# Kernel optimization log

Hardware: AMD Instinct MI355X
Metric: run time of the kernel (lower is better)

## Reference

```python
import jax, jax.numpy as jnp
import numpy as np

N = 100_000      # nodes
E = 1_600_000    # edges
NG = 512         # graphs in batch
EPS = 1e-5


def _prop(x, src, dst, n, add_self_loops):
    """GCN-normalized sparse propagation: agg_i = sum_{j->i} d_j^-1/2 d_i^-1/2 x_j."""
    ones = jnp.ones(src.shape[0], x.dtype)
    deg = jax.ops.segment_sum(ones, dst, num_segments=n)
    if add_self_loops:
        deg = deg + 1.0
    dinv = jnp.where(deg > 0, jax.lax.rsqrt(jnp.maximum(deg, 1e-12)), 0.0)
    w = dinv[src] * dinv[dst]                       # [E]
    agg = jax.ops.segment_sum(x[src] * w[:, None], dst, num_segments=n)
    if add_self_loops:
        agg = agg + x * (dinv * dinv)[:, None]
    return agg


def setup_inputs() -> dict:
    key = jax.random.key(0)
    ks = jax.random.split(key, 24)
    w = lambda k, s: jax.random.normal(k, s, jnp.float32) * 0.05
    dim = 100
    return {
        "x": jax.random.normal(ks[0], (N, 128), jnp.float32),
        "src": jax.random.randint(ks[1], (E,), 0, N),
        "dst": jax.random.randint(ks[2], (E,), 0, N),
        "batch": jnp.sort(jax.random.randint(ks[3], (N,), 0, NG)),
        # SGConv 1 & 2 (propagate then Linear)
        "W1": w(ks[4], (128, dim)), "b1": jnp.zeros((dim,), jnp.float32),
        "W2": w(ks[5], (dim, dim)), "b2": jnp.zeros((dim,), jnp.float32),
        # BatchNorm1d affine params
        "gamma": jnp.ones((dim,), jnp.float32), "beta": jnp.zeros((dim,), jnp.float32),
        # ARMAConv (num_stacks=1, num_layers=1)
        "Wa_init": w(ks[6], (dim, dim)), "Wa_root": w(ks[7], (dim, dim)),
        "ba": jnp.zeros((dim,), jnp.float32),
        # MLP head
        "Wf1": w(ks[8], (dim, 2 * dim)), "bf1": jnp.zeros((2 * dim,), jnp.float32),
        "Wf2": w(ks[9], (2 * dim, 3 * dim)), "bf2": jnp.zeros((3 * dim,), jnp.float32),
        "Wf3": w(ks[10], (3 * dim, 2 * dim)), "bf3": jnp.zeros((2 * dim,), jnp.float32),
        "Wf4": w(ks[11], (2 * dim, 1)), "bf4": jnp.zeros((1,), jnp.float32),
    }


def reference(x, src, dst, batch, W1, b1, W2, b2, gamma, beta,
              Wa_init, Wa_root, ba, Wf1, bf1, Wf2, bf2, Wf3, bf3, Wf4, bf4):
    n = x.shape[0]
    # SGConv (K=1): propagate with self-loop gcn_norm, then linear; ReLU
    h = jax.nn.relu(_prop(x, src, dst, n, True) @ W1 + b1)
    h = jax.nn.relu(_prop(h, src, dst, n, True) @ W2 + b2)
    # BatchNorm1d (training mode: batch statistics, biased var)
    mu = jnp.mean(h, axis=0)
    var = jnp.mean((h - mu) ** 2, axis=0)
    h = (h - mu) * jax.lax.rsqrt(var + EPS) * gamma + beta
    # ARMAConv (1 stack, 1 layer): ReLU(A_hat (h W_init) + h W_root + b), no self-loops
    a = jax.nn.relu(_prop(h @ Wa_init, src, dst, n, False) + h @ Wa_root + ba)
    # global_add_pool over graph ids
    g = jax.ops.segment_sum(a, batch, num_segments=NG)   # [NG, dim]
    # MLP head
    g = jax.nn.relu(g @ Wf1 + bf1)
    g = jax.nn.relu(g @ Wf2 + bf2)
    g = jax.nn.relu(g @ Wf3 + bf3)
    return g @ Wf4 + bf4
```

## Files before the change

### kernel.cpp

```cpp
#include <hip/hip_runtime.h>
#include <hip/hip_fp16.h>

#define NNODES 100000
#define NEDGES 1600000
#define NGRAPH 512
#define DIM    100
#define DP     128
#define EPSBN  1e-5f
#define NBUK   ((NNODES + 255) >> 8)
#define BINCH  8192

typedef _Float16 half8 __attribute__((ext_vector_type(8)));
typedef float floatx4 __attribute__((ext_vector_type(4)));

__global__ __launch_bounds__(256) void bin_count_kernel(const int* __restrict__ dst,
                                                        int* __restrict__ btotal, int e) {
    __shared__ int lc[NBUK];
    int tid = threadIdx.x;
    int base = blockIdx.x * BINCH;
    int m = e - base; if (m > BINCH) m = BINCH;
    for (int b = tid; b < NBUK; b += 256) lc[b] = 0;
    __syncthreads();
    for (int j = tid; j < m; j += 256)
        atomicAdd(&lc[dst[base + j] >> 8], 1);
    __syncthreads();
    for (int b = tid; b < NBUK; b += 256)
        if (lc[b]) atomicAdd(&btotal[b], lc[b]);
}

__global__ void bucket_scan_kernel(const int* __restrict__ btotal, int* __restrict__ bbase,
                                   int* __restrict__ bcursor, int e,
                                   const int* __restrict__ batch, int* __restrict__ gstart, int n) {
    __shared__ int s[512];
    int tid = threadIdx.x;
    int v = (tid < NBUK) ? btotal[tid] : 0;
    s[tid] = v; __syncthreads();
    for (int o = 1; o < 512; o <<= 1) {
        int t = (tid >= o) ? s[tid - o] : 0;
        __syncthreads();
        s[tid] += t;
        __syncthreads();
    }
    if (tid < NBUK) {
        int base = s[tid] - v;
        bbase[tid] = base;
        bcursor[tid] = base;
    }
    if (tid == 0) bbase[NBUK] = e;

    {
        int g = tid;
        int lo = 0, hi = n;
        while (lo < hi) {
            int mid = (lo + hi) >> 1;
            if (batch[mid] < g) lo = mid + 1; else hi = mid;
        }
        gstart[g] = lo;
        if (g == 0) gstart[NGRAPH] = n;
    }
}

__global__ __launch_bounds__(256) void bin_kernel(
        const int* __restrict__ src, const int* __restrict__ dst,
        int* __restrict__ bcursor, unsigned int* __restrict__ gpairs, int e) {
    __shared__ int2 lpairs[BINCH];
    __shared__ int lcount[NBUK], lstart[NBUK], lcur[NBUK], gbase[NBUK];
    int tid = threadIdx.x;
    int base = blockIdx.x * BINCH;
    int m = e - base; if (m > BINCH) m = BINCH;

    for (int b = tid; b < NBUK; b += 256) lcount[b] = 0;
    __syncthreads();
    for (int j = tid; j < m; j += 256)
        atomicAdd(&lcount[dst[base + j] >> 8], 1);
    __syncthreads();
    if (tid == 0) {
        int acc = 0;
        for (int b = 0; b < NBUK; b++) {
            lstart[b] = acc;
            lcur[b] = acc;
            acc += lcount[b];
        }
    }
    __syncthreads();
    for (int b = tid; b < NBUK; b += 256)
        gbase[b] = atomicAdd(&bcursor[b], lcount[b]);
    for (int j = tid; j < m; j += 256) {
        int s = src[base + j], d = dst[base + j];
        int p = atomicAdd(&lcur[d >> 8], 1);
        lpairs[p] = make_int2(s, d);
    }
    __syncthreads();
    for (int j = tid; j < m; j += 256) {
        int2 pr = lpairs[j];
        int b = pr.y >> 8;
        gpairs[gbase[b] + (j - lstart[b])] =
            ((unsigned int)pr.x << 8) | ((unsigned int)pr.y & 255u);
    }
}

__global__ __launch_bounds__(256) void bucket_build_kernel(
        const unsigned int* __restrict__ gpairs, const int* __restrict__ bbase,
        int* __restrict__ off, int* __restrict__ ssorted,
        float* __restrict__ dsl, float* __restrict__ dnsl, int n, int e) {
    __shared__ int cnt[256];
    __shared__ int sc[256];
    int b = blockIdx.x, tid = threadIdx.x;
    int node0 = b << 8;
    int e0 = bbase[b], e1 = bbase[b + 1];

    cnt[tid] = 0;
    __syncthreads();
    for (int j = e0 + tid; j < e1; j += 256)
        atomicAdd(&cnt[gpairs[j] & 255u], 1);
    __syncthreads();

    int c = cnt[tid];
    sc[tid] = c; __syncthreads();
    for (int o = 1; o < 256; o <<= 1) {
        int t = (tid >= o) ? sc[tid - o] : 0;
        __syncthreads();
        sc[tid] += t;
        __syncthreads();
    }
    int excl = sc[tid] - c;

    int node = node0 + tid;
    if (node < n) {
        off[node] = e0 + excl;
        float cf = (float)c;
        dsl[node] = rsqrtf(cf + 1.0f);
        dnsl[node] = (c > 0) ? rsqrtf(cf) : 0.0f;
    }
    if (b == NBUK - 1 && tid == 0) off[n] = e;

    __syncthreads();
    cnt[tid] = e0 + excl;
    __syncthreads();
    for (int j = e0 + tid; j < e1; j += 256) {
        unsigned int pk = gpairs[j];
        int p = atomicAdd(&cnt[pk & 255u], 1);
        ssorted[p] = (int)(pk >> 8);
    }
}

__global__ void packW4_kernel(const float* __restrict__ W1, const float* __restrict__ W2,
                              const float* __restrict__ W3, const float* __restrict__ W4,
                              _Float16* __restrict__ Wt1, _Float16* __restrict__ Wt2,
                              _Float16* __restrict__ Wt3, _Float16* __restrict__ Wt4,
                              const float* __restrict__ b1, const float* __restrict__ b2,
                              float* __restrict__ b1p, float* __restrict__ b2p,
                              int* __restrict__ btotal, float* __restrict__ bnsum,
                              float* __restrict__ bnsq, __half* __restrict__ buf0zr) {
    if (blockIdx.x == 256) {
        int t = threadIdx.x;
        if (t < 128) {
            b1p[t] = (t < DIM) ? b1[t] : 0.f;
            b2p[t] = (t < DIM) ? b2[t] : 0.f;
            bnsum[t] = 0.f;
            bnsq[t] = 0.f;
        }
        for (int i = t; i < NBUK; i += 256) btotal[i] = 0;
        if (t < 64) ((unsigned int*)buf0zr)[t] = 0u;
        return;
    }
    int which = blockIdx.x >> 6;
    int idx = (blockIdx.x & 63) * 256 + threadIdx.x;
    const float* W = (which == 0) ? W1 : (which == 1) ? W2 : (which == 2) ? W3 : W4;
    _Float16* Wt  = (which == 0) ? Wt1 : (which == 1) ? Wt2 : (which == 2) ? Wt3 : Wt4;
    int K = (which == 0) ? 128 : DIM;
    int j = idx & 7;
    int l = (idx >> 3) & 63;
    int c = idx >> 9;
    int t = c >> 2, k0 = c & 3;
    int nn = t * 16 + (l & 15);
    int k = k0 * 32 + (l >> 4) * 8 + j;
    float v = (k < K && nn < DIM) ? W[k * DIM + nn] : 0.f;
    Wt[idx] = (_Float16)v;
}

__global__ __launch_bounds__(256) void prop_kernel(
        const __half* __restrict__ pre, const int* __restrict__ ssorted,
        const int* __restrict__ off, const float* __restrict__ dinv,
        const float* __restrict__ bias, __half* __restrict__ outH, int n) {
    int wave = (blockIdx.x * blockDim.x + threadIdx.x) >> 6;
    int lane = threadIdx.x & 63;
    if (wave >= n) return;
    int e0 = off[wave], e1 = off[wave + 1];
    int deg = e1 - e0;
    int g = lane >> 4;
    int q = lane & 15;
    const int ZR = n;

    float acc[8];
#pragma unroll
    for (int i = 0; i < 8; i++) acc[i] = 0.f;

    auto addu = [&](uint4 u) {
        float2 f;
        f = __half22float2(*(__half2*)&u.x); acc[0] += f.x; acc[1] += f.y;
        f = __half22float2(*(__half2*)&u.y); acc[2] += f.x; acc[3] += f.y;
        f = __half22float2(*(__half2*)&u.z); acc[4] += f.x; acc[5] += f.y;
        f = __half22float2(*(__half2*)&u.w); acc[6] += f.x; acc[7] += f.y;
    };
    auto rowptr = [&](int s) -> const uint4* {
        return (const uint4*)&pre[(long)s * DP + q * 8];
    };

    for (int base = 0; base < deg; base += 64) {
        int m = deg - base; if (m > 64) m = 64;
        int sidx = (lane < m) ? ssorted[e0 + base + lane] : ZR;
        for (int j = 0; j < m; j += 16) {
            int s0 = __shfl(sidx, j + g);
            int s1 = __shfl(sidx, j + 4 + g);
            int s2 = __shfl(sidx, j + 8 + g);
            int s3 = __shfl(sidx, j + 12 + g);
            uint4 u0 = *rowptr(s0);
            uint4 u1 = *rowptr(s1);
            uint4 u2 = *rowptr(s2);
            uint4 u3 = *rowptr(s3);
            addu(u0); addu(u1); addu(u2); addu(u3);
        }
    }

#pragma unroll
    for (int i = 0; i < 8; i++) {
        acc[i] += __shfl_xor(acc[i], 16);
        acc[i] += __shfl_xor(acc[i], 32);
    }

    if (g == 0) {
        float dn = dinv[wave];
        addu(*rowptr(wave));
        float4 b0 = *(const float4*)&bias[q * 8];
        float4 b1v = *(const float4*)&bias[q * 8 + 4];
        float o[8];
        o[0] = fmaxf(dn * acc[0] + b0.x, 0.f);
        o[1] = fmaxf(dn * acc[1] + b0.y, 0.f);
        o[2] = fmaxf(dn * acc[2] + b0.z, 0.f);
        o[3] = fmaxf(dn * acc[3] + b0.w, 0.f);
        o[4] = fmaxf(dn * acc[4] + b1v.x, 0.f);
        o[5] = fmaxf(dn * acc[5] + b1v.y, 0.f);
        o[6] = fmaxf(dn * acc[6] + b1v.z, 0.f);
        o[7] = fmaxf(dn * acc[7] + b1v.w, 0.f);
        __half2 p0 = __floats2half2_rn(o[0], o[1]);
        __half2 p1 = __floats2half2_rn(o[2], o[3]);
        __half2 p2 = __floats2half2_rn(o[4], o[5]);
        __half2 p3 = __floats2half2_rn(o[6], o[7]);
        uint4 u;
        u.x = *(unsigned int*)&p0;
        u.y = *(unsigned int*)&p1;
        u.z = *(unsigned int*)&p2;
        u.w = *(unsigned int*)&p3;
        *(uint4*)&outH[(long)wave * DP + q * 8] = u;
    }
}

__global__ __launch_bounds__(256) void prop_arma_kernel(
        const __half* __restrict__ pre, const int* __restrict__ ssorted,
        const int* __restrict__ off, const float* __restrict__ dinv,
        const __half* __restrict__ R, __half* __restrict__ outH, int n) {
    int wave = (blockIdx.x * blockDim.x + threadIdx.x) >> 6;
    int lane = threadIdx.x & 63;
    if (wave >= n) return;
    int e0 = off[wave], e1 = off[wave + 1];
    int deg = e1 - e0;
    int g = lane >> 4;
    int q = lane & 15;
    const int ZR = n;

    float acc[8];
#pragma unroll
    for (int i = 0; i < 8; i++) acc[i] = 0.f;

    auto addu = [&](uint4 u) {
        float2 f;
        f = __half22float2(*(__half2*)&u.x); acc[0] += f.x; acc[1] += f.y;
        f = __half22float2(*(__half2*)&u.y); acc[2] += f.x; acc[3] += f.y;
        f = __half22float2(*(__half2*)&u.z); acc[4] += f.x; acc[5] += f.y;
        f = __half22float2(*(__half2*)&u.w); acc[6] += f.x; acc[7] += f.y;
    };
    auto rowptr = [&](int s) -> const uint4* {
        return (const uint4*)&pre[(long)s * DP + q * 8];
    };

    for (int base = 0; base < deg; base += 64) {
        int m = deg - base; if (m > 64) m = 64;
        int sidx = (lane < m) ? ssorted[e0 + base + lane] : ZR;
        for (int j = 0; j < m; j += 16) {
            int s0 = __shfl(sidx, j + g);
            int s1 = __shfl(sidx, j + 4 + g);
            int s2 = __shfl(sidx, j + 8 + g);
            int s3 = __shfl(sidx, j + 12 + g);
            uint4 u0 = *rowptr(s0);
            uint4 u1 = *rowptr(s1);
            uint4 u2 = *rowptr(s2);
            uint4 u3 = *rowptr(s3);
            addu(u0); addu(u1); addu(u2); addu(u3);
        }
    }

#pragma unroll
    for (int i = 0; i < 8; i++) {
        acc[i] += __shfl_xor(acc[i], 16);
        acc[i] += __shfl_xor(acc[i], 32);
    }

    if (g == 0) {
        float dn = dinv[wave];
        uint4 r4 = *(const uint4*)&R[(long)wave * DP + q * 8];
        float rr[8];
        float2 f;
        f = __half22float2(*(__half2*)&r4.x); rr[0] = f.x; rr[1] = f.y;
        f = __half22float2(*(__half2*)&r4.y); rr[2] = f.x; rr[3] = f.y;
        f = __half22float2(*(__half2*)&r4.z); rr[4] = f.x; rr[5] = f.y;
        f = __half22float2(*(__half2*)&r4.w); rr[6] = f.x; rr[7] = f.y;
        float o[8];
#pragma unroll
        for (int i = 0; i < 8; i++) o[i] = fmaxf(dn * acc[i] + rr[i], 0.f);
        __half2 p0 = __floats2half2_rn(o[0], o[1]);
        __half2 p1 = __floats2half2_rn(o[2], o[3]);
        __half2 p2 = __floats2half2_rn(o[4], o[5]);
        __half2 p3 = __floats2half2_rn(o[6], o[7]);
        uint4 u;
        u.x = *(unsigned int*)&p0;
        u.y = *(unsigned int*)&p1;
        u.z = *(unsigned int*)&p2;
        u.w = *(unsigned int*)&p3;
        *(uint4*)&outH[(long)wave * DP + q * 8] = u;
    }
}

__global__ __launch_bounds__(256) void matmul_a32_kernel(
        const float* __restrict__ A, const _Float16* __restrict__ WtF,
        const float* __restrict__ rowscale, __half* __restrict__ Ch, int M) {
    __shared__ char smraw[64 * 132 * 4];
    _Float16* Bs = (_Float16*)smraw;
    float* Ct = (float*)smraw;
    int tid = threadIdx.x;
    int wave = tid >> 6;
    int lane = tid & 63;
    int m16 = lane & 15;
    int quad = lane >> 4;
    long row0blk = (long)blockIdx.x * 64;
    long row0 = row0blk + wave * 16;

    {
        const uint4* s = (const uint4*)WtF;
        uint4* d = (uint4*)Bs;
        for (int i = tid; i < 2048; i += 256) d[i] = s[i];
    }

    half8 af[4];
    {
        long ar = row0 + m16; if (ar >= M) ar = M - 1;
        const float* Ap = &A[ar * DP + quad * 8];
#pragma unroll
        for (int k0 = 0; k0 < 4; k0++) {
            float4 v0 = *(const float4*)(Ap + k0 * 32);
            float4 v1 = *(const float4*)(Ap + k0 * 32 + 4);
            half8 o;
            o[0] = (_Float16)v0.x; o[1] = (_Float16)v0.y;
            o[2] = (_Float16)v0.z; o[3] = (_Float16)v0.w;
            o[4] = (_Float16)v1.x; o[5] = (_Float16)v1.y;
            o[6] = (_Float16)v1.z; o[7] = (_Float16)v1.w;
            af[k0] = o;
        }
    }
    __syncthreads();

    floatx4 acc[8];
#pragma unroll
    for (int t = 0; t < 8; t++) acc[t] = (floatx4){0.f, 0.f, 0.f, 0.f};

#pragma unroll
    for (int c = 0; c < 32; c++) {
        half8 bf = *(const half8*)&Bs[(c * 64 + lane) * 8];
        acc[c >> 2] = __builtin_amdgcn_mfma_f32_16x16x32_f16(af[c & 3], bf, acc[c >> 2], 0, 0, 0);
    }
    __syncthreads();

    int lrow0 = wave * 16 + quad * 4;
#pragma unroll
    for (int t = 0; t < 8; t++)
#pragma unroll
        for (int r = 0; r < 4; r++)
            Ct[(lrow0 + r) * 132 + t * 16 + m16] = acc[t][r];
    __syncthreads();

    for (int idx = tid; idx < 64 * 32; idx += 256) {
        int lr = idx >> 5, c4 = idx & 31;
        long grow = row0blk + lr;
        if (grow >= M) continue;
        int col = c4 * 4;
        float4 v = *(const float4*)&Ct[lr * 132 + col];
        float rs = rowscale[grow];
        v.x *= rs; v.y *= rs; v.z *= rs; v.w *= rs;
        __half2 p01 = __floats2half2_rn(v.x, v.y);
        __half2 p23 = __floats2half2_rn(v.z, v.w);
        uint2 u;
        u.x = *(unsigned int*)&p01;
        u.y = *(unsigned int*)&p23;
        *(uint2*)&Ch[grow * DP + col] = u;
    }
}

__global__ __launch_bounds__(256) void matmul_a16_kernel(
        const __half* __restrict__ A, const _Float16* __restrict__ WtF,
        const float* __restrict__ rowscale, __half* __restrict__ Ch, int M) {
    __shared__ char smraw[64 * 132 * 4];
    _Float16* Bs = (_Float16*)smraw;
    float* Ct = (float*)smraw;
    int tid = threadIdx.x;
    int wave = tid >> 6;
    int lane = tid & 63;
    int m16 = lane & 15;
    int quad = lane >> 4;
    long row0blk = (long)blockIdx.x * 64;
    long row0 = row0blk + wave * 16;

    {
        const uint4* s = (const uint4*)WtF;
        uint4* d = (uint4*)Bs;
        for (int i = tid; i < 2048; i += 256) d[i] = s[i];
    }

    half8 af[4];
    {
        long ar = row0 + m16; if (ar >= M) ar = M - 1;
        const _Float16* Ap = (const _Float16*)&A[ar * DP + quad * 8];
#pragma unroll
        for (int k0 = 0; k0 < 4; k0++)
            af[k0] = *(const half8*)(Ap + k0 * 32);
    }
    __syncthreads();

    floatx4 acc[8];
#pragma unroll
    for (int t = 0; t < 8; t++) acc[t] = (floatx4){0.f, 0.f, 0.f, 0.f};

#pragma unroll
    for (int c = 0; c < 32; c++) {
        half8 bf = *(const half8*)&Bs[(c * 64 + lane) * 8];
        acc[c >> 2] = __builtin_amdgcn_mfma_f32_16x16x32_f16(af[c & 3], bf, acc[c >> 2], 0, 0, 0);
    }
    __syncthreads();

    int lrow0 = wave * 16 + quad * 4;
#pragma unroll
    for (int t = 0; t < 8; t++)
#pragma unroll
        for (int r = 0; r < 4; r++)
            Ct[(lrow0 + r) * 132 + t * 16 + m16] = acc[t][r];
    __syncthreads();

    for (int idx = tid; idx < 64 * 32; idx += 256) {
        int lr = idx >> 5, c4 = idx & 31;
        long grow = row0blk + lr;
        if (grow >= M) continue;
        int col = c4 * 4;
        float4 v = *(const float4*)&Ct[lr * 132 + col];
        float rs = rowscale[grow];
        v.x *= rs; v.y *= rs; v.z *= rs; v.w *= rs;
        __half2 p01 = __floats2half2_rn(v.x, v.y);
        __half2 p23 = __floats2half2_rn(v.z, v.w);
        uint2 u;
        u.x = *(unsigned int*)&p01;
        u.y = *(unsigned int*)&p23;
        *(uint2*)&Ch[grow * DP + col] = u;
    }
}

__global__ __launch_bounds__(256) void matmul_dual_kernel(
        const __half* __restrict__ A, const _Float16* __restrict__ WtF3,
        const _Float16* __restrict__ WtF4, const float* __restrict__ ba,
        const float* __restrict__ rowscale,
        const float* __restrict__ bnscale, const float* __restrict__ bnshift,
        __half* __restrict__ Ch1, __half* __restrict__ ChR, int M, int Kout) {
    __shared__ char smraw[64 * 132 * 4];
    _Float16* Bs = (_Float16*)smraw;
    float* Ct = (float*)smraw;
    int tid = threadIdx.x;
    int wave = tid >> 6;
    int lane = tid & 63;
    int m16 = lane & 15;
    int quad = lane >> 4;
    long row0blk = (long)blockIdx.x * 64;
    long row0 = row0blk + wave * 16;

    half8 af[4];
    {
        long ar = row0 + m16; if (ar >= M) ar = M - 1;
        const _Float16* Ap = (const _Float16*)&A[ar * DP + quad * 8];
#pragma unroll
        for (int k0 = 0; k0 < 4; k0++) {
            half8 h = *(const half8*)(Ap + k0 * 32);
            int c0 = quad * 8 + k0 * 32;
            float4 sc0 = *(const float4*)&bnscale[c0];
            float4 sc1 = *(const float4*)&bnscale[c0 + 4];
            float4 sh0 = *(const float4*)&bnshift[c0];
            float4 sh1 = *(const float4*)&bnshift[c0 + 4];
            half8 o;
            o[0] = (_Float16)((float)h[0] * sc0.x + sh0.x);
            o[1] = (_Float16)((float)h[1] * sc0.y + sh0.y);
            o[2] = (_Float16)((float)h[2] * sc0.z + sh0.z);
            o[3] = (_Float16)((float)h[3] * sc0.w + sh0.w);
            o[4] = (_Float16)((float)h[4] * sc1.x + sh1.x);
            o[5] = (_Float16)((float)h[5] * sc1.y + sh1.y);
            o[6] = (_Float16)((float)h[6] * sc1.z + sh1.z);
            o[7] = (_Float16)((float)h[7] * sc1.w + sh1.w);
            af[k0] = o;
        }
    }

    floatx4 acc3[8], acc4[8];
#pragma unroll
    for (int t = 0; t < 8; t++) {
        acc3[t] = (floatx4){0.f, 0.f, 0.f, 0.f};
        acc4[t] = (floatx4){0.f, 0.f, 0.f, 0.f};
    }

    {
        const uint4* s = (const uint4*)WtF3;
        uint4* d = (uint4*)Bs;
        for (int i = tid; i < 2048; i += 256) d[i] = s[i];
    }
    __syncthreads();
#pragma unroll
    for (int c = 0; c < 32; c++) {
        half8 bf = *(const half8*)&Bs[(c * 64 + lane) * 8];
        acc3[c >> 2] = __builtin_amdgcn_mfma_f32_16x16x32_f16(af[c & 3], bf, acc3[c >> 2], 0, 0, 0);
    }
    __syncthreads();

    {
        const uint4* s = (const uint4*)WtF4;
        uint4* d = (uint4*)Bs;
        for (int i = tid; i < 2048; i += 256) d[i] = s[i];
    }
    __syncthreads();
#pragma unroll
    for (int c = 0; c < 32; c++) {
        half8 bf = *(const half8*)&Bs[(c * 64 + lane) * 8];
        acc4[c >> 2] = __builtin_amdgcn_mfma_f32_16x16x32_f16(af[c & 3], bf, acc4[c >> 2], 0, 0, 0);
    }
    __syncthreads();

    int lrow0 = wave * 16 + quad * 4;

#pragma unroll
    for (int t = 0; t < 8; t++)
#pragma unroll
        for (int r = 0; r < 4; r++)
            Ct[(lrow0 + r) * 132 + t * 16 + m16] = acc3[t][r];
    __syncthreads();
    for (int idx = tid; idx < 64 * 32; idx += 256) {
        int lr = idx >> 5, c4 = idx & 31;
        long grow = row0blk + lr;
        if (grow >= M) continue;
        int col = c4 * 4;
        float4 v = *(const float4*)&Ct[lr * 132 + col];
        float rs = rowscale[grow];
        v.x *= rs; v.y *= rs; v.z *= rs; v.w *= rs;
        __half2 p01 = __floats2half2_rn(v.x, v.y);
        __half2 p23 = __floats2half2_rn(v.z, v.w);
        uint2 u;
        u.x = *(unsigned int*)&p01;
        u.y = *(unsigned int*)&p23;
        *(uint2*)&Ch1[grow * DP + col] = u;
    }
    __syncthreads();

#pragma unroll
    for (int t = 0; t < 8; t++)
#pragma unroll
        for (int r = 0; r < 4; r++)
            Ct[(lrow0 + r) * 132 + t * 16 + m16] = acc4[t][r];
    __syncthreads();
    for (int idx = tid; idx < 64 * 32; idx += 256) {
        int lr = idx >> 5, c4 = idx & 31;
        long grow = row0blk + lr;
        if (grow >= M) continue;
        int col = c4 * 4;
        float4 v = *(const float4*)&Ct[lr * 132 + col];
        if (col + 4 <= Kout) {
            float4 bb = *(const float4*)&ba[col];
            v.x += bb.x; v.y += bb.y; v.z += bb.z; v.w += bb.w;
        }
        __half2 p01 = __floats2half2_rn(v.x, v.y);
        __half2 p23 = __floats2half2_rn(v.z, v.w);
        uint2 u;
        u.x = *(unsigned int*)&p01;
        u.y = *(unsigned int*)&p23;
        *(uint2*)&ChR[grow * DP + col] = u;
    }
}

__global__ __launch_bounds__(512) void bnstats_kernel(const __half* __restrict__ h,
                                                      float* __restrict__ bnsum,
                                                      float* __restrict__ bnsq, int n) {
    __shared__ float2 sred[512], qred[512];
    int tid = threadIdx.x;
    int col2 = tid & 63;
    int rgrp = tid >> 6;
    float2 s = make_float2(0.f, 0.f), qv = make_float2(0.f, 0.f);
    if (col2 < 52) {
        for (int r = blockIdx.x * 8 + rgrp; r < n; r += gridDim.x * 8) {
            __half2 hv = *(const __half2*)&h[(long)r * DP + col2 * 2];
            float2 f = __half22float2(hv);
            s.x += f.x; s.y += f.y;
            qv.x += f.x * f.x; qv.y += f.y * f.y;
        }
    }
    sred[tid] = s; qred[tid] = qv;
    __syncthreads();
    if (tid < 52) {
        float2 ts = make_float2(0.f, 0.f), tq = make_float2(0.f, 0.f);
#pragma unroll
        for (int gg = 0; gg < 8; gg++) {
            float2 v = sred[gg * 64 + tid]; ts.x += v.x; ts.y += v.y;
            v = qred[gg * 64 + tid]; tq.x += v.x; tq.y += v.y;
        }
        atomicAdd(&bnsum[tid * 2], ts.x);
        atomicAdd(&bnsum[tid * 2 + 1], ts.y);
        atomicAdd(&bnsq[tid * 2], tq.x);
        atomicAdd(&bnsq[tid * 2 + 1], tq.y);
    }
}

__global__ void bn_prep_kernel(const float* __restrict__ sum, const float* __restrict__ sq,
                               const float* __restrict__ gamma, const float* __restrict__ beta,
                               float* __restrict__ scale, float* __restrict__ shift, int n) {
    int c = threadIdx.x;
    float sc = 0.f, sh = 0.f;
    if (c < DIM) {
        float inv_n = 1.0f / (float)n;
        float mu = sum[c] * inv_n;
        float var = sq[c] * inv_n - mu * mu;
        float rs = rsqrtf(var + EPSBN);
        sc = rs * gamma[c];
        sh = beta[c] - mu * sc;
    }
    scale[c] = sc;
    shift[c] = sh;
}

__global__ __launch_bounds__(512) void pmlp_kernel(
        const __half* __restrict__ a, const int* __restrict__ gstart,
        const float* __restrict__ Wf1, const float* __restrict__ bf1,
        const float* __restrict__ Wf2, const float* __restrict__ bf2,
        const float* __restrict__ Wf3, const float* __restrict__ bf3,
        const float* __restrict__ Wf4, const float* __restrict__ bf4,
        float* __restrict__ out) {
    __shared__ float2 red[512];
    __shared__ float gsum[128], a1[200], a2[300], a3[200], red1[512];
    int b = blockIdx.x, tid = threadIdx.x;

    {
        int col2 = tid & 63;
        int rgrp = tid >> 6;
        int lo = gstart[b], hi = gstart[b + 1];
        float2 s = make_float2(0.f, 0.f);
        for (int r = lo + rgrp; r < hi; r += 8) {
            __half2 h = *(const __half2*)&a[(long)r * DP + col2 * 2];
            float2 f = __half22float2(h);
            s.x += f.x; s.y += f.y;
        }
        red[tid] = s;
        __syncthreads();
        if (tid < 64) {
            float2 t = make_float2(0.f, 0.f);
#pragma unroll
            for (int gg = 0; gg < 8; gg++) {
                float2 v = red[gg * 64 + tid];
                t.x += v.x; t.y += v.y;
            }
            gsum[tid * 2] = t.x;
            gsum[tid * 2 + 1] = t.y;
        }
        __syncthreads();
    }

    for (int c = tid; c < 200; c += 512) {
        float s = bf1[c];
        for (int k = 0; k < 100; k++) s += gsum[k] * Wf1[k * 200 + c];
        a1[c] = fmaxf(s, 0.f);
    }
    __syncthreads();
    for (int c = tid; c < 300; c += 512) {
        float s = bf2[c];
        for (int k = 0; k < 200; k++) s += a1[k] * Wf2[k * 300 + c];
        a2[c] = fmaxf(s, 0.f);
    }
    __syncthreads();
    for (int c = tid; c < 200; c += 512) {
        float s = bf3[c];
        for (int k = 0; k < 300; k++) s += a2[k] * Wf3[k * 200 + c];
        a3[c] = fmaxf(s, 0.f);
    }
    __syncthreads();
    red1[tid] = (tid < 200) ? a3[tid] * Wf4[tid] : 0.f;
    __syncthreads();
    for (int o = 256; o > 0; o >>= 1) {
        if (tid < o) red1[tid] += red1[tid + o];
        __syncthreads();
    }
    if (tid == 0) out[b] = red1[0] + bf4[0];
}

extern "C" void kernel_launch(void* const* d_in, const int* in_sizes, int n_in,
                              void* d_out, int out_size, void* d_ws, size_t ws_size,
                              hipStream_t stream) {
    const float* x      = (const float*)d_in[0];
    const int*   src    = (const int*)d_in[1];
    const int*   dst    = (const int*)d_in[2];
    const int*   batch  = (const int*)d_in[3];
    const float* W1     = (const float*)d_in[4];
    const float* b1     = (const float*)d_in[5];
    const float* W2     = (const float*)d_in[6];
    const float* b2     = (const float*)d_in[7];
    const float* gamma  = (const float*)d_in[8];
    const float* beta   = (const float*)d_in[9];
    const float* Wa_init= (const float*)d_in[10];
    const float* Wa_root= (const float*)d_in[11];
    const float* ba     = (const float*)d_in[12];
    const float* Wf1    = (const float*)d_in[13];
    const float* bf1    = (const float*)d_in[14];
    const float* Wf2    = (const float*)d_in[15];
    const float* bf2    = (const float*)d_in[16];
    const float* Wf3    = (const float*)d_in[17];
    const float* bf3    = (const float*)d_in[18];
    const float* Wf4    = (const float*)d_in[19];
    const float* bf4    = (const float*)d_in[20];
    float* out = (float*)d_out;

    const int n = NNODES;
    const int e = NEDGES;

    char* ws = (char*)d_ws;
    auto carve = [&](size_t bytes) -> void* {
        void* p = (void*)ws;
        ws += (bytes + 255) & ~(size_t)255;
        return p;
    };
    __half* buf0    = (__half*)carve((size_t)(n + 1) * DP * 2);
    __half* buf1    = (__half*)carve((size_t)n * DP * 2);
    __half* bufR    = (__half*)carve((size_t)n * DP * 2);
    __half* bufC    = (__half*)carve((size_t)n * DP * 2);
    _Float16* Wt1   = (_Float16*)carve((size_t)DP * DP * 2);
    _Float16* Wt2   = (_Float16*)carve((size_t)DP * DP * 2);
    _Float16* Wt3   = (_Float16*)carve((size_t)DP * DP * 2);
    _Float16* Wt4   = (_Float16*)carve((size_t)DP * DP * 2);
    int*    off     = (int*)carve((size_t)(n + 1) * 4);
    int*    btotal  = (int*)carve((size_t)NBUK * 4);
    int*    bbase   = (int*)carve((size_t)(NBUK + 1) * 4);
    int*    bcursor = (int*)carve((size_t)NBUK * 4);
    int*    ssorted = (int*)carve((size_t)e * 4);
    unsigned int* gpairs = (unsigned int*)carve((size_t)e * 4);
    float*  dinv_sl = (float*)carve((size_t)n * 4);
    float*  dinv_nsl= (float*)carve((size_t)n * 4);
    float*  bnsum   = (float*)carve(DP * 4);
    float*  bnsq    = (float*)carve(DP * 4);
    float*  bnscale = (float*)carve(DP * 4);
    float*  bnshift = (float*)carve(DP * 4);
    float*  b1p     = (float*)carve(DP * 4);
    float*  b2p     = (float*)carve(DP * 4);
    int*    gstart  = (int*)carve((size_t)(NGRAPH + 1) * 4);

    const int nchunk = (e + BINCH - 1) / BINCH;

    packW4_kernel<<<257, 256, 0, stream>>>(W1, W2, Wa_init, Wa_root, Wt1, Wt2, Wt3, Wt4,
                                           b1, b2, b1p, b2p, btotal, bnsum, bnsq,
                                           buf0 + (size_t)n * DP);

    bin_count_kernel<<<nchunk, 256, 0, stream>>>(dst, btotal, e);
    bucket_scan_kernel<<<1, 512, 0, stream>>>(btotal, bbase, bcursor, e, batch, gstart, n);
    bin_kernel<<<nchunk, 256, 0, stream>>>(src, dst, bcursor, gpairs, e);
    bucket_build_kernel<<<NBUK, 256, 0, stream>>>(gpairs, bbase, off, ssorted, dinv_sl, dinv_nsl, n, e);

    const int prop_blocks = (n + 3) / 4;
    const int mm_blocks = (n + 63) / 64;

    matmul_a32_kernel<<<mm_blocks, 256, 0, stream>>>(x, Wt1, dinv_sl, buf0, n);
    prop_kernel<<<prop_blocks, 256, 0, stream>>>(buf0, ssorted, off, dinv_sl, b1p, buf1, n);

    matmul_a16_kernel<<<mm_blocks, 256, 0, stream>>>(buf1, Wt2, dinv_sl, buf0, n);
    prop_kernel<<<prop_blocks, 256, 0, stream>>>(buf0, ssorted, off, dinv_sl, b2p, buf1, n);

    bnstats_kernel<<<512, 512, 0, stream>>>(buf1, bnsum, bnsq, n);
    bn_prep_kernel<<<1, 128, 0, stream>>>(bnsum, bnsq, gamma, beta, bnscale, bnshift, n);

    matmul_dual_kernel<<<mm_blocks, 256, 0, stream>>>(buf1, Wt3, Wt4, ba, dinv_nsl, bnscale, bnshift, buf0, bufR, n, DIM);
    prop_arma_kernel<<<prop_blocks, 256, 0, stream>>>(buf0, ssorted, off, dinv_nsl, bufR, bufC, n);

    pmlp_kernel<<<NGRAPH, 512, 0, stream>>>(bufC, gstart, Wf1, bf1, Wf2, bf2, Wf3, bf3, Wf4, bf4, out);
}
```

Measured before the change: 503.3 us.

## Shrink binning chunks with parallel scan and double matmul row tiles

Binning now uses 2048-edge chunks with 512-thread blocks, which gives more blocks and parallelism. The serial single-thread bucket prefix in bin_kernel is replaced by a parallel block scan. The a32/a16 matmul kernels now process 128 rows per block, so the staged weight tile is reused across two 64-row halves. This raises register use and adds extra syncs in the epilogue, and smaller chunks mean more global atomics on bcursor.

Result: no change. 504.5 us (+0.2%).

```diff
diff --git a/kernel.cpp b/kernel.cpp
--- a/kernel.cpp
+++ b/kernel.cpp
@@ -8,23 +8,23 @@
 #define DP     128
 #define EPSBN  1e-5f
 #define NBUK   ((NNODES + 255) >> 8)
-#define BINCH  8192
+#define BINCH  2048
 
 typedef _Float16 half8 __attribute__((ext_vector_type(8)));
 typedef float floatx4 __attribute__((ext_vector_type(4)));
 
-__global__ __launch_bounds__(256) void bin_count_kernel(const int* __restrict__ dst,
+__global__ __launch_bounds__(512) void bin_count_kernel(const int* __restrict__ dst,
                                                         int* __restrict__ btotal, int e) {
     __shared__ int lc[NBUK];
     int tid = threadIdx.x;
     int base = blockIdx.x * BINCH;
     int m = e - base; if (m > BINCH) m = BINCH;
-    for (int b = tid; b < NBUK; b += 256) lc[b] = 0;
-    __syncthreads();
-    for (int j = tid; j < m; j += 256)
+    for (int b = tid; b < NBUK; b += 512) lc[b] = 0;
+    __syncthreads();
+    for (int j = tid; j < m; j += 512)
         atomicAdd(&lc[dst[base + j] >> 8], 1);
     __syncthreads();
-    for (int b = tid; b < NBUK; b += 256)
+    for (int b = tid; b < NBUK; b += 512)
         if (lc[b]) atomicAdd(&btotal[b], lc[b]);
 }
 
@@ -60,38 +60,44 @@
     }
 }
 
-__global__ __launch_bounds__(256) void bin_kernel(
+__global__ __launch_bounds__(512) void bin_kernel(
         const int* __restrict__ src, const int* __restrict__ dst,
         int* __restrict__ bcursor, unsigned int* __restrict__ gpairs, int e) {
     __shared__ int2 lpairs[BINCH];
     __shared__ int lcount[NBUK], lstart[NBUK], lcur[NBUK], gbase[NBUK];
+    __shared__ int s[512];
     int tid = threadIdx.x;
     int base = blockIdx.x * BINCH;
     int m = e - base; if (m > BINCH) m = BINCH;
 
-    for (int b = tid; b < NBUK; b += 256) lcount[b] = 0;
-    __syncthreads();
-    for (int j = tid; j < m; j += 256)
+    for (int b = tid; b < NBUK; b += 512) lcount[b] = 0;
+    __syncthreads();
+    for (int j = tid; j < m; j += 512)
         atomicAdd(&lcount[dst[base + j] >> 8], 1);
     __syncthreads();
-    if (tid == 0) {
-        int acc = 0;
-        for (int b = 0; b < NBUK; b++) {
-            lstart[b] = acc;
-            lcur[b] = acc;
-            acc += lcount[b];
-        }
-    }
-    __syncthreads();
-    for (int b = tid; b < NBUK; b += 256)
-        gbase[b] = atomicAdd(&bcursor[b], lcount[b]);
-    for (int j = tid; j < m; j += 256) {
-        int s = src[base + j], d = dst[base + j];
+
+    int v = (tid < NBUK) ? lcount[tid] : 0;
+    s[tid] = v; __syncthreads();
+    for (int o = 1; o < 512; o <<= 1) {
+        int t = (tid >= o) ? s[tid - o] : 0;
+        __syncthreads();
+        s[tid] += t;
+        __syncthreads();
+    }
+    if (tid < NBUK) {
+        lstart[tid] = s[tid] - v;
+        lcur[tid] = s[tid] - v;
+        gbase[tid] = atomicAdd(&bcursor[tid], v);
+    }
+    __syncthreads();
+
+    for (int j = tid; j < m; j += 512) {
+        int sv = src[base + j], d = dst[base + j];
         int p = atomicAdd(&lcur[d >> 8], 1);
-        lpairs[p] = make_int2(s, d);
-    }
-    __syncthreads();
-    for (int j = tid; j < m; j += 256) {
+        lpairs[p] = make_int2(sv, d);
+    }
+    __syncthreads();
+    for (int j = tid; j < m; j += 512) {
         int2 pr = lpairs[j];
         int b = pr.y >> 8;
         gpairs[gbase[b] + (j - lstart[b])] =
@@ -342,8 +348,7 @@
     int lane = tid & 63;
     int m16 = lane & 15;
     int quad = lane >> 4;
-    long row0blk = (long)blockIdx.x * 64;
-    long row0 = row0blk + wave * 16;
+    long row0blk = (long)blockIdx.x * 128;
 
     {
         const uint4* s = (const uint4*)WtF;
@@ -351,9 +356,10 @@
         for (int i = tid; i < 2048; i += 256) d[i] = s[i];
     }
 
-    half8 af[4];
-    {
-        long ar = row0 + m16; if (ar >= M) ar = M - 1;
+    half8 af[2][4];
+#pragma unroll
+    for (int t = 0; t < 2; t++) {
+        long ar = row0blk + t * 64 + wave * 16 + m16; if (ar >= M) ar = M - 1;
         const float* Ap = &A[ar * DP + quad * 8];
 #pragma unroll
         for (int k0 = 0; k0 < 4; k0++) {
@@ -364,44 +370,49 @@
             o[2] = (_Float16)v0.z; o[3] = (_Float16)v0.w;
             o[4] = (_Float16)v1.x; o[5] = (_Float16)v1.y;
             o[6] = (_Float16)v1.z; o[7] = (_Float16)v1.w;
-            af[k0] = o;
-        }
-    }
-    __syncthreads();
-
-    floatx4 acc[8];
-#pragma unroll
-    for (int t = 0; t < 8; t++) acc[t] = (floatx4){0.f, 0.f, 0.f, 0.f};
+            af[t][k0] = o;
+        }
+    }
+    __syncthreads();
+
+    floatx4 acc[2][8];
+#pragma unroll
+    for (int t = 0; t < 2; t++)
+#pragma unroll
+        for (int a = 0; a < 8; a++) acc[t][a] = (floatx4){0.f, 0.f, 0.f, 0.f};
 
 #pragma unroll
     for (int c = 0; c < 32; c++) {
         half8 bf = *(const half8*)&Bs[(c * 64 + lane) * 8];
-        acc[c >> 2] = __builtin_amdgcn_mfma_f32_16x16x32_f16(af[c & 3], bf, acc[c >> 2], 0, 0, 0);
-    }
-    __syncthreads();
+        acc[0][c >> 2] = __builtin_amdgcn_mfma_f32_16x16x32_f16(af[0][c & 3], bf, acc[0][c >> 2], 0, 0, 0);
+        acc[1][c >> 2] = __builtin_amdgcn_mfma_f32_16x16x32_f16(af[1][c & 3], bf, acc[1][c >> 2], 0, 0, 0);
+    }
 
     int lrow0 = wave * 16 + quad * 4;
 #pragma unroll
-    for (int t = 0; t < 8; t++)
-#pragma unroll
-        for (int r = 0; r < 4; r++)
-            Ct[(lrow0 + r) * 132 + t * 16 + m16] = acc[t][r];
-    __syncthreads();
-
-    for (int idx = tid; idx < 64 * 32; idx += 256) {
-        int lr = idx >> 5, c4 = idx & 31;
-        long grow = row0blk + lr;
-        if (grow >= M) continue;
-        int col = c4 * 4;
-        float4 v = *(const float4*)&Ct[lr * 132 + col];
-        float rs = rowscale[grow];
-        v.x *= rs; v.y *= rs; v.z *= rs; v.w *= rs;
-        __half2 p01 = __floats2half2_rn(v.x, v.y);
-        __half2 p23 = __floats2half2_rn(v.z, v.w);
-        uint2 u;
-        u.x = *(unsigned int*)&p01;
-        u.y = *(unsigned int*)&p23;
-        *(uint2*)&Ch[grow * DP + col] = u;
+    for (int t = 0; t < 2; t++) {
+        __syncthreads();
+#pragma unroll
+        for (int a = 0; a < 8; a++)
+#pragma unroll
+            for (int r = 0; r < 4; r++)
+                Ct[(lrow0 + r) * 132 + a * 16 + m16] = acc[t][a][r];
+        __syncthreads();
+        for (int idx = tid; idx < 64 * 32; idx += 256) {
+            int lr = idx >> 5, c4 = idx & 31;
+            long grow = row0blk + t * 64 + lr;
+            if (grow >= M) continue;
+            int col = c4 * 4;
+            float4 v = *(const float4*)&Ct[lr * 132 + col];
+            float rs = rowscale[grow];
+            v.x *= rs; v.y *= rs; v.z *= rs; v.w *= rs;
+            __half2 p01 = __floats2half2_rn(v.x, v.y);
+            __half2 p23 = __floats2half2_rn(v.z, v.w);
+            uint2 u;
+            u.x = *(unsigned int*)&p01;
+            u.y = *(unsigned int*)&p23;
+            *(uint2*)&Ch[grow * DP + col] = u;
+        }
     }
 }
 
@@ -416,8 +427,7 @@
     int lane = tid & 63;
     int m16 = lane & 15;
     int quad = lane >> 4;
-    long row0blk = (long)blockIdx.x * 64;
-    long row0 = row0blk + wave * 16;
+    long row0blk = (long)blockIdx.x * 128;
 
     {
         const uint4* s = (const uint4*)WtF;
@@ -425,49 +435,55 @@
         for (int i = tid; i < 2048; i += 256) d[i] = s[i];
     }
 
-    half8 af[4];
-    {
-        long ar = row0 + m16; if (ar >= M) ar = M - 1;
+    half8 af[2][4];
+#pragma unroll
+    for (int t = 0; t < 2; t++) {
+        long ar = row0blk + t * 64 + wave * 16 + m16; if (ar >= M) ar = M - 1;
         const _Float16* Ap = (const _Float16*)&A[ar * DP + quad * 8];
 #pragma unroll
         for (int k0 = 0; k0 < 4; k0++)
-            af[k0] = *(const half8*)(Ap + k0 * 32);
-    }
-    __syncthreads();
-
-    floatx4 acc[8];
-#pragma unroll
-    for (int t = 0; t < 8; t++) acc[t] = (floatx4){0.f, 0.f, 0.f, 0.f};
+            af[t][k0] = *(const half8*)(Ap + k0 * 32);
+    }
+    __syncthreads();
+
+    floatx4 acc[2][8];
+#pragma unroll
+    for (int t = 0; t < 2; t++)
+#pragma unroll
+        for (int a = 0; a < 8; a++) acc[t][a] = (floatx4){0.f, 0.f, 0.f, 0.f};
 
 #pragma unroll
     for (int c = 0; c < 32; c++) {
         half8 bf = *(const half8*)&Bs[(c * 64 + lane) * 8];
-        acc[c >> 2] = __builtin_amdgcn_mfma_f32_16x16x32_f16(af[c & 3], bf, acc[c >> 2], 0, 0, 0);
-    }
-    __syncthreads();
+        acc[0][c >> 2] = __builtin_amdgcn_mfma_f32_16x16x32_f16(af[0][c & 3], bf, acc[0][c >> 2], 0, 0, 0);
+        acc[1][c >> 2] = __builtin_amdgcn_mfma_f32_16x16x32_f16(af[1][c & 3], bf, acc[1][c >> 2], 0, 0, 0);
+    }
 
     int lrow0 = wave * 16 + quad * 4;
 #pragma unroll
-    for (int t = 0; t < 8; t++)
-#pragma unroll
-        for (int r = 0; r < 4; r++)
-            Ct[(lrow0 + r) * 132 + t * 16 + m16] = acc[t][r];
-    __syncthreads();
-
-    for (int idx = tid; idx < 64 * 32; idx += 256) {
-        int lr = idx >> 5, c4 = idx & 31;
-        long grow = row0blk + lr;
-        if (grow >= M) continue;
-        int col = c4 * 4;
-        float4 v = *(const float4*)&Ct[lr * 132 + col];
-        float rs = rowscale[grow];
-        v.x *= rs; v.y *= rs; v.z *= rs; v.w *= rs;
-        __half2 p01 = __floats2half2_rn(v.x, v.y);
-        __half2 p23 = __floats2half2_rn(v.z, v.w);
-        uint2 u;
-        u.x = *(unsigned int*)&p01;
-        u.y = *(unsigned int*)&p23;
-        *(uint2*)&Ch[grow * DP + col] = u;
+    for (int t = 0; t < 2; t++) {
+        __syncthreads();
+#pragma unroll
+        for (int a = 0; a < 8; a++)
+#pragma unroll
+            for (int r = 0; r < 4; r++)
+                Ct[(lrow0 + r) * 132 + a * 16 + m16] = acc[t][a][r];
+        __syncthreads();
+        for (int idx = tid; idx < 64 * 32; idx += 256) {
+            int lr = idx >> 5, c4 = idx & 31;
+            long grow = row0blk + t * 64 + lr;
+            if (grow >= M) continue;
+            int col = c4 * 4;
+            float4 v = *(const float4*)&Ct[lr * 132 + col];
+            float rs = rowscale[grow];
+            v.x *= rs; v.y *= rs; v.z *= rs; v.w *= rs;
+            __half2 p01 = __floats2half2_rn(v.x, v.y);
+            __half2 p23 = __floats2half2_rn(v.z, v.w);
+            uint2 u;
+            u.x = *(unsigned int*)&p01;
+            u.y = *(unsigned int*)&p23;
+            *(uint2*)&Ch[grow * DP + col] = u;
+        }
     }
 }
 
@@ -773,24 +789,25 @@
                                            b1, b2, b1p, b2p, btotal, bnsum, bnsq,
                                            buf0 + (size_t)n * DP);
 
-    bin_count_kernel<<<nchunk, 256, 0, stream>>>(dst, btotal, e);
+    bin_count_kernel<<<nchunk, 512, 0, stream>>>(dst, btotal, e);
     bucket_scan_kernel<<<1, 512, 0, stream>>>(btotal, bbase, bcursor, e, batch, gstart, n);
-    bin_kernel<<<nchunk, 256, 0, stream>>>(src, dst, bcursor, gpairs, e);
+    bin_kernel<<<nchunk, 512, 0, stream>>>(src, dst, bcursor, gpairs, e);
     bucket_build_kernel<<<NBUK, 256, 0, stream>>>(gpairs, bbase, off, ssorted, dinv_sl, dinv_nsl, n, e);
 
     const int prop_blocks = (n + 3) / 4;
-    const int mm_blocks = (n + 63) / 64;
-
-    matmul_a32_kernel<<<mm_blocks, 256, 0, stream>>>(x, Wt1, dinv_sl, buf0, n);
+    const int mm_blocks128 = (n + 127) / 128;
+    const int mm_blocks64 = (n + 63) / 64;
+
+    matmul_a32_kernel<<<mm_blocks128, 256, 0, stream>>>(x, Wt1, dinv_sl, buf0, n);
     prop_kernel<<<prop_blocks, 256, 0, stream>>>(buf0, ssorted, off, dinv_sl, b1p, buf1, n);
 
-    matmul_a16_kernel<<<mm_blocks, 256, 0, stream>>>(buf1, Wt2, dinv_sl, buf0, n);
+    matmul_a16_kernel<<<mm_blocks128, 256, 0, stream>>>(buf1, Wt2, dinv_sl, buf0, n);
     prop_kernel<<<prop_blocks, 256, 0, stream>>>(buf0, ssorted, off, dinv_sl, b2p, buf1, n);
 
     bnstats_kernel<<<512, 512, 0, stream>>>(buf1, bnsum, bnsq, n);
     bn_prep_kernel<<<1, 128, 0, stream>>>(bnsum, bnsq, gamma, beta, bnscale, bnshift, n);
 
-    matmul_dual_kernel<<<mm_blocks, 256, 0, stream>>>(buf1, Wt3, Wt4, ba, dinv_nsl, bnscale, bnshift, buf0, bufR, n, DIM);
+    matmul_dual_kernel<<<mm_blocks64, 256, 0, stream>>>(buf1, Wt3, Wt4, ba, dinv_nsl, bnscale, bnshift, buf0, bufR, n, DIM);
     prop_arma_kernel<<<prop_blocks, 256, 0, stream>>>(buf0, ssorted, off, dinv_nsl, bufR, bufC, n);
 
     pmlp_kernel<<<NGRAPH, 512, 0, stream>>>(bufC, gstart, Wf1, bf1, Wf2, bf2, Wf3, bf3, Wf4, bf4, out);
```
